# Kernel optimization log

Hardware: AMD Instinct MI355X
Metric: run time of the kernel (lower is better)

The kernel has to match this reference:

```python
import jax, jax.numpy as jnp
import numpy as np

SEQ_LEN = 8192
D_MODEL = 1024
D_K = 128
D_V = 128


def setup_inputs() -> dict:
    key = jax.random.key(0)
    kx, kq, kk, kv = jax.random.split(key, 4)
    # xavier-uniform scale for (out, in) linear weights
    def xavier(k, out_f, in_f):
        lim = np.sqrt(6.0 / (in_f + out_f))
        return jax.random.uniform(k, (out_f, in_f), jnp.float32, -lim, lim)
    return {
        "X": jax.random.normal(kx, (SEQ_LEN, D_MODEL), jnp.float32),
        "Wq": xavier(kq, D_K, D_MODEL),
        "Wk": xavier(kk, D_K, D_MODEL),
        "Wv": xavier(kv, D_V, D_MODEL),
    }


def reference(X, Wq, Wk, Wv):
    # X: (S, d_model); W*: (d_k, d_model) torch Linear weights (y = x @ W.T)
    S = X.shape[0]
    Q = X @ Wq.T                      # (S, d_k)
    K = X @ Wk.T                      # (S, d_k)
    V = X @ Wv.T                      # (S, d_v)
    scale = jnp.sqrt(jnp.asarray(D_K, X.dtype))
    scores = (Q @ K.T) / scale        # (S, S)
    causal = jnp.tril(jnp.ones((S, S), bool))
    scores = jnp.where(causal, scores, -jnp.inf)
    weights = jax.nn.softmax(scores, axis=1)
    # dropout p=0.0 -> identity
    Z = weights @ V                   # (S, d_v)
    return Z
```

## Files before the change

### kernel.cpp

```cpp
#include <hip/hip_runtime.h>
#include <hip/hip_bf16.h>

#define S_LEN 8192
#define DM    1024
#define DK    128
#define KSTR  136
#define VSTR  72
#define SLOTD 1056

typedef __attribute__((ext_vector_type(8))) short bf16x8;
typedef __attribute__((ext_vector_type(8))) _Float16 f16x8;
typedef __attribute__((ext_vector_type(4))) float f32x4;

__device__ __forceinline__ f32x4 mfma16(bf16x8 a, bf16x8 b, f32x4 c) {
    return __builtin_amdgcn_mfma_f32_16x16x32_bf16(a, b, c, 0, 0, 0);
}
__device__ __forceinline__ f32x4 mfma16f(f16x8 a, f16x8 b, f32x4 c) {
    return __builtin_amdgcn_mfma_f32_16x16x32_f16(a, b, c, 0, 0, 0);
}

__device__ __forceinline__ ushort f2bf(float f) {
    unsigned u = __builtin_bit_cast(unsigned, f);
    u += 0x7FFFu + ((u >> 16) & 1u);
    return (ushort)(u >> 16);
}

__device__ __forceinline__ ushort f2h(float f) {
    return __builtin_bit_cast(ushort, (_Float16)f);
}

__device__ __forceinline__ uint cvt_pk_bf16(float a, float b) {
    uint r;
    asm("v_cvt_pk_bf16_f32 %0, %1, %2" : "=v"(r) : "v"(a), "v"(b));
    return r;
}

__global__ __launch_bounds__(256, 1)
void convert_w_kernel(const float* __restrict__ Wq,
                      const float* __restrict__ Wk,
                      const float* __restrict__ Wv,
                      _Float16* __restrict__ Wh) {
    const int NW4 = DK * DM / 4;
    const int i = blockIdx.x * 256 + threadIdx.x;
    const int which = i / NW4;
    const int off = i - which * NW4;
    const float4 v = ((const float4*)(which == 0 ? Wq : (which == 1 ? Wk : Wv)))[off];
    union { _Float16 h[4]; uint2 u; } p;
    p.h[0] = (_Float16)v.x; p.h[1] = (_Float16)v.y;
    p.h[2] = (_Float16)v.z; p.h[3] = (_Float16)v.w;
    *(uint2*)(Wh + (size_t)which * (DK * DM) + (size_t)off * 4) = p.u;
}

__global__ __launch_bounds__(256)
void proj_gemm_kernel(const float* __restrict__ X,
                      const _Float16* __restrict__ Wh,
                      ushort* __restrict__ Qb,
                      ushort* __restrict__ Kb,
                      ushort* __restrict__ Vtb) {
    __shared__ _Float16 Ash[32 * 32];
    __shared__ _Float16 Bsh[128 * 32];

    const int tid  = threadIdx.x;
    const int lane = tid & 63;
    const int quad = lane >> 4;
    const int l15  = lane & 15;
    const int wv   = tid >> 6;
    const int wm   = wv & 1;
    const int wn   = wv >> 1;
    const int m0   = blockIdx.x * 32;
    const int nb   = blockIdx.y;
    const _Float16* Wbase = Wh + nb * (DK * DM);
    const int arow = tid >> 3, ac4 = tid & 7;

    f32x4 acc[4];
#pragma unroll
    for (int ni = 0; ni < 4; ++ni) acc[ni] = (f32x4){0.f, 0.f, 0.f, 0.f};

    float4 ra = *(const float4*)(X + (size_t)(m0 + arow) * DM + ac4 * 4);

    for (int kk = 0; kk < DM; kk += 32) {
        __syncthreads();
        for (int s = tid; s < 512; s += 256) {
            const int row = s >> 2, sg = s & 3;
            __builtin_amdgcn_global_load_lds(
                (const __attribute__((address_space(1))) void*)(Wbase + (size_t)row * DM + kk + sg * 8),
                (__attribute__((address_space(3))) void*)(Bsh + s * 8), 16, 0, 0);
        }
        {
            union { _Float16 h[4]; uint2 u; } pa;
            pa.h[0] = (_Float16)ra.x; pa.h[1] = (_Float16)ra.y;
            pa.h[2] = (_Float16)ra.z; pa.h[3] = (_Float16)ra.w;
            *(uint2*)(Ash + arow * 32 + ac4 * 4) = pa.u;
        }
        if (kk + 32 < DM)
            ra = *(const float4*)(X + (size_t)(m0 + arow) * DM + kk + 32 + ac4 * 4);
        __syncthreads();

        const f16x8 af = *(const f16x8*)(Ash + (wm * 16 + l15) * 32 + quad * 8);
        f16x8 bf[4];
#pragma unroll
        for (int t = 0; t < 4; ++t)
            bf[t] = *(const f16x8*)(Bsh + (wn * 64 + t * 16 + l15) * 32 + quad * 8);
#pragma unroll
        for (int ni = 0; ni < 4; ++ni)
            acc[ni] = mfma16f(af, bf[ni], acc[ni]);
    }

    if (nb == 2) {
#pragma unroll
        for (int ni = 0; ni < 4; ++ni) {
            const int n = wn * 64 + ni * 16 + l15;
            const int m = m0 + wm * 16 + quad * 4;
            union { ushort h[4]; uint2 u; } p;
#pragma unroll
            for (int r = 0; r < 4; ++r) p.h[r] = f2bf(acc[ni][r]);
            *(uint2*)(Vtb + (size_t)n * S_LEN + m) = p.u;
        }
    } else {
        ushort* Ob = (nb == 0) ? Qb : Kb;
        const float sc = (nb == 0) ? 0.088388347648318447f * 1.4426950408889634f : 1.0f;
#pragma unroll
        for (int ni = 0; ni < 4; ++ni) {
            const int n = wn * 64 + ni * 16 + l15;
#pragma unroll
            for (int r = 0; r < 4; ++r) {
                const int m = m0 + wm * 16 + quad * 4 + r;
                Ob[(size_t)m * DK + n] = f2bf(acc[ni][r] * sc);
            }
        }
    }
}

__global__ __launch_bounds__(256, 3)
void flash_partial_kernel(const ushort* __restrict__ Qg,
                          const ushort* __restrict__ Kg,
                          const ushort* __restrict__ Vtg,
                          float* __restrict__ Part) {
    __shared__ __align__(16) ushort Ks [64 * KSTR];
    __shared__ __align__(16) ushort Vts[128 * VSTR];

    const int b = 995 - (int)blockIdx.x;
    int qb, chunk;
    if (b < 36) {
        int q = 0;
        while (b >= (q + 1) * (q + 2) / 2) ++q;
        qb = q; chunk = b - q * (q + 1) / 2;
    } else {
        qb = 8 + ((b - 36) >> 3);
        chunk = (b - 36) & 7;
    }
    const int nkt   = qb + 1;
    const int NC    = nkt < 8 ? nkt : 8;
    const int kt_lo = chunk * nkt / NC;
    const int kt_hi = (chunk + 1) * nkt / NC;

    const int tid  = threadIdx.x;
    const int wv   = tid >> 6;
    const int lane = tid & 63;
    const int quad = lane >> 4;
    const int l15  = lane & 15;
    const int q0w  = qb * 64 + wv * 16;

    bf16x8 qf[4];
    {
        const ushort* qrow = Qg + (size_t)(q0w + l15) * DK + quad * 8;
#pragma unroll
        for (int kc = 0; kc < 4; ++kc) qf[kc] = *(const bf16x8*)(qrow + kc * 32);
    }

    float m_ = -__builtin_inff();
    float l_ = 0.f;
    f32x4 acc[8];
#pragma unroll
    for (int d = 0; d < 8; ++d) acc[d] = (f32x4){0.f, 0.f, 0.f, 0.f};

    bf16x8 stg[8];
#define LOAD_TILE(K0)                                                          \
    {                                                                          \
        const int k0_ = (K0);                                                  \
        _Pragma("unroll")                                                      \
        for (int i = 0; i < 8; ++i) {                                          \
            const int c = tid + (i << 8);                                      \
            if (c < 1024) {                                                    \
                const int row = c >> 4, ch = c & 15;                           \
                stg[i] = *(const bf16x8*)(Kg + (size_t)(k0_ + row) * DK + ch * 8); \
            } else {                                                           \
                const int cc = c - 1024;                                       \
                const int row = cc >> 3, ch = cc & 7;                          \
                stg[i] = *(const bf16x8*)(Vtg + (size_t)row * S_LEN + k0_ + ch * 8); \
            }                                                                  \
        }                                                                      \
    }

    LOAD_TILE(kt_lo * 64)

    for (int kt = kt_lo; kt < kt_hi; ++kt) {
        const int k0 = kt * 64;

        __syncthreads();
#pragma unroll
        for (int i = 0; i < 8; ++i) {
            const int c = tid + (i << 8);
            if (c < 1024) {
                const int row = c >> 4, ch = c & 15;
                *(bf16x8*)(Ks + row * KSTR + ch * 8) = stg[i];
            } else {
                const int cc = c - 1024;
                const int row = cc >> 3, ch = cc & 7;
                const int s_lo = ((ch >> 2) << 5) + ((ch & 1) << 4) + (((ch >> 1) & 1) << 2);
                union { bf16x8 v; uint2 q2[2]; } u;
                u.v = stg[i];
                ushort* vb = Vts + row * VSTR + s_lo;
                *(uint2*)vb       = u.q2[0];
                *(uint2*)(vb + 8) = u.q2[1];
            }
        }
        if (kt + 1 < kt_hi) LOAD_TILE((kt + 1) * 64)
        __syncthreads();

        f32x4 Sr[4];
        __builtin_amdgcn_s_setprio(1);
#pragma unroll
        for (int nb = 0; nb < 4; ++nb) {
            Sr[nb] = (f32x4){0.f, 0.f, 0.f, 0.f};
            const ushort* kb = Ks + (nb * 16 + l15) * KSTR + quad * 8;
#pragma unroll
            for (int kc = 0; kc < 4; ++kc)
                Sr[nb] = mfma16(*(const bf16x8*)(kb + kc * 32), qf[kc], Sr[nb]);
        }
        __builtin_amdgcn_s_setprio(0);

        if (k0 + 63 > q0w) {
            const int qg = q0w + l15;
#pragma unroll
            for (int nb = 0; nb < 4; ++nb) {
                const int kg = k0 + nb * 16 + quad * 4;
#pragma unroll
                for (int r = 0; r < 4; ++r)
                    if (kg + r > qg) Sr[nb][r] = -__builtin_inff();
            }
        }

        float pmax;
        {
            float a0 = fmaxf(fmaxf(Sr[0][0], Sr[0][1]), fmaxf(Sr[0][2], Sr[0][3]));
            float a1 = fmaxf(fmaxf(Sr[1][0], Sr[1][1]), fmaxf(Sr[1][2], Sr[1][3]));
            float a2 = fmaxf(fmaxf(Sr[2][0], Sr[2][1]), fmaxf(Sr[2][2], Sr[2][3]));
            float a3 = fmaxf(fmaxf(Sr[3][0], Sr[3][1]), fmaxf(Sr[3][2], Sr[3][3]));
            pmax = fmaxf(fmaxf(a0, a1), fmaxf(a2, a3));
            pmax = fmaxf(pmax, __shfl_xor(pmax, 16));
            pmax = fmaxf(pmax, __shfl_xor(pmax, 32));
        }
        if (__any(pmax > m_ + 8.f)) {
            const float mnew = fmaxf(m_, pmax);
            const float al = __builtin_amdgcn_exp2f(m_ - mnew);
            m_ = mnew;
            l_ *= al;
            float alr[4];
#pragma unroll
            for (int r = 0; r < 4; ++r)
                alr[r] = __shfl(al, (lane & 48) | (((lane >> 4) & 3) * 4 + r));
#pragma unroll
            for (int d = 0; d < 8; ++d)
#pragma unroll
                for (int r = 0; r < 4; ++r) acc[d][r] *= alr[r];
        }

        float p[4][4];
        float rs = 0.f;
#pragma unroll
        for (int nb = 0; nb < 4; ++nb)
#pragma unroll
            for (int r = 0; r < 4; ++r) {
                p[nb][r] = __builtin_amdgcn_exp2f(Sr[nb][r] - m_);
                rs += p[nb][r];
            }
        rs += __shfl_xor(rs, 16);
        rs += __shfl_xor(rs, 32);
        l_ += rs;

        __builtin_amdgcn_s_setprio(1);
#pragma unroll
        for (int kcp = 0; kcp < 2; ++kcp) {
            union { uint u[4]; bf16x8 v; } pf;
            pf.u[0] = cvt_pk_bf16(p[2 * kcp][0],     p[2 * kcp][1]);
            pf.u[1] = cvt_pk_bf16(p[2 * kcp][2],     p[2 * kcp][3]);
            pf.u[2] = cvt_pk_bf16(p[2 * kcp + 1][0], p[2 * kcp + 1][1]);
            pf.u[3] = cvt_pk_bf16(p[2 * kcp + 1][2], p[2 * kcp + 1][3]);
#pragma unroll
            for (int db = 0; db < 8; ++db) {
                const bf16x8 vf = *(const bf16x8*)(Vts + (db * 16 + l15) * VSTR + kcp * 32 + quad * 8);
                acc[db] = mfma16(pf.v, vf, acc[db]);
            }
        }
        __builtin_amdgcn_s_setprio(0);
    }
#undef LOAD_TILE

    const int qt16 = qb * 4 + wv;
    float* slot = Part + (size_t)(qt16 * 8 + chunk) * SLOTD;
    if (quad == 0) {
        slot[l15]      = m_;
        slot[16 + l15] = l_;
    }
    uint* slotO = (uint*)(slot + 32);
#pragma unroll
    for (int d = 0; d < 8; ++d)
#pragma unroll
        for (int r = 0; r < 4; ++r) {
            const float v  = acc[d][r];
            const float vp = __shfl_xor(v, 1);
            if ((l15 & 1) == 0) {
                const int row = quad * 4 + r;
                const uint u = (uint)f2h(v) | ((uint)f2h(vp) << 16);
                slotO[(row * 128 + d * 16 + l15) >> 1] = u;
            }
        }
}

__global__ __launch_bounds__(256)
void flash_merge_kernel(const float* __restrict__ Part, float* __restrict__ Out) {
    __shared__ float Ms[16], Ls[16];
    __shared__ float Sc[8][16];
    const int qt = blockIdx.x;
    const int q0 = qt * 16;
    const int qb = qt >> 2;
    const int P  = (qb + 1 < 8) ? (qb + 1) : 8;
    const int tid = threadIdx.x;
    const float* base = Part + (size_t)qt * 8 * SLOTD;

    if (tid < 16) {
        float M = -__builtin_inff();
        for (int p = 0; p < P; ++p) M = fmaxf(M, base[p * SLOTD + tid]);
        float L = 0.f;
        for (int p = 0; p < P; ++p)
            L += base[p * SLOTD + 16 + tid] * exp2f(base[p * SLOTD + tid] - M);
        Ms[tid] = M; Ls[tid] = L;
    }
    __syncthreads();
    if (tid < 128) {
        const int p = tid >> 4, row = tid & 15;
        Sc[p][row] = (p < P) ? exp2f(base[p * SLOTD + row] - Ms[row]) : 0.f;
    }
    __syncthreads();

#pragma unroll
    for (int j = tid; j < 1024; j += 256) {
        const int row = j >> 6, c2 = j & 63;
        float o0 = 0.f, o1 = 0.f;
        for (int p = 0; p < P; ++p) {
            const uint u = ((const uint*)(base + p * SLOTD + 32))[row * 64 + c2];
            const float sc = Sc[p][row];
            o0 += (float)__builtin_bit_cast(_Float16, (ushort)(u & 0xFFFF)) * sc;
            o1 += (float)__builtin_bit_cast(_Float16, (ushort)(u >> 16)) * sc;
        }
        const float inv = 1.0f / Ls[row];
        float2 o; o.x = o0 * inv; o.y = o1 * inv;
        *(float2*)(Out + (size_t)(q0 + row) * DK + c2 * 2) = o;
    }
}

extern "C" void kernel_launch(void* const* d_in, const int* in_sizes, int n_in,
                              void* d_out, int out_size, void* d_ws, size_t ws_size,
                              hipStream_t stream) {
    const float* X  = (const float*)d_in[0];
    const float* Wq = (const float*)d_in[1];
    const float* Wk = (const float*)d_in[2];
    const float* Wv = (const float*)d_in[3];
    ushort* ws  = (ushort*)d_ws;
    ushort* Qb  = ws;
    ushort* Kb  = ws + (size_t)S_LEN * DK;
    ushort* Vtb = ws + 2 * (size_t)S_LEN * DK;
    _Float16* Wh = (_Float16*)(ws + 3 * (size_t)S_LEN * DK);
    float* Part = (float*)(Wh + (size_t)3 * DK * DM);
    float* Out = (float*)d_out;

    convert_w_kernel<<<384, 256, 0, stream>>>(Wq, Wk, Wv, Wh);
    proj_gemm_kernel<<<dim3(256, 3), 256, 0, stream>>>(X, Wh, Qb, Kb, Vtb);
    flash_partial_kernel<<<996, 256, 0, stream>>>(Qb, Kb, Vtb, Part);
    flash_merge_kernel<<<512, 256, 0, stream>>>(Part, Out);
}
```

Before: 148.8 us.

## Register-prefetch X and W tiles with K=64 steps and padded LDS in projection GEMM

```diff
diff --git a/kernel.cpp b/kernel.cpp
--- a/kernel.cpp
+++ b/kernel.cpp
@@ -6,6 +6,7 @@
 #define DK    128
 #define KSTR  136
 #define VSTR  72
+#define ASTR  68
 #define SLOTD 1056
 
 typedef __attribute__((ext_vector_type(8))) short bf16x8;
@@ -57,8 +58,8 @@
                       ushort* __restrict__ Qb,
                       ushort* __restrict__ Kb,
                       ushort* __restrict__ Vtb) {
-    __shared__ _Float16 Ash[32 * 32];
-    __shared__ _Float16 Bsh[128 * 32];
+    __shared__ _Float16 Ash[32 * ASTR];
+    __shared__ _Float16 Bsh[128 * ASTR];
 
     const int tid  = threadIdx.x;
     const int lane = tid & 63;
@@ -70,41 +71,65 @@
     const int m0   = blockIdx.x * 32;
     const int nb   = blockIdx.y;
     const _Float16* Wbase = Wh + nb * (DK * DM);
-    const int arow = tid >> 3, ac4 = tid & 7;
 
     f32x4 acc[4];
 #pragma unroll
     for (int ni = 0; ni < 4; ++ni) acc[ni] = (f32x4){0.f, 0.f, 0.f, 0.f};
 
-    float4 ra = *(const float4*)(X + (size_t)(m0 + arow) * DM + ac4 * 4);
-
-    for (int kk = 0; kk < DM; kk += 32) {
+    float4 sa[2];
+    f16x8 sb[4];
+
+#define LOADR(KK)                                                              \
+    {                                                                          \
+        _Pragma("unroll")                                                      \
+        for (int i = 0; i < 2; ++i) {                                          \
+            const int s = tid + (i << 8);                                      \
+            sa[i] = *(const float4*)(X + (size_t)(m0 + (s >> 4)) * DM + (KK) + (s & 15) * 4); \
+        }                                                                      \
+        _Pragma("unroll")                                                      \
+        for (int i = 0; i < 4; ++i) {                                          \
+            const int s = tid + (i << 8);                                      \
+            sb[i] = *(const f16x8*)(Wbase + (size_t)(s >> 3) * DM + (KK) + (s & 7) * 8); \
+        }                                                                      \
+    }
+#define WRITE_LDS()                                                            \
+    {                                                                          \
+        _Pragma("unroll")                                                      \
+        for (int i = 0; i < 2; ++i) {                                          \
+            const int s = tid + (i << 8);                                      \
+            union { _Float16 h[4]; uint2 u; } pa_;                             \
+            pa_.h[0] = (_Float16)sa[i].x; pa_.h[1] = (_Float16)sa[i].y;        \
+            pa_.h[2] = (_Float16)sa[i].z; pa_.h[3] = (_Float16)sa[i].w;        \
+            *(uint2*)(Ash + (s >> 4) * ASTR + (s & 15) * 4) = pa_.u;           \
+        }                                                                      \
+        _Pragma("unroll")                                                      \
+        for (int i = 0; i < 4; ++i) {                                          \
+            const int s = tid + (i << 8);                                      \
+            *(f16x8*)(Bsh + (s >> 3) * ASTR + (s & 7) * 8) = sb[i];            \
+        }                                                                      \
+    }
+
+    LOADR(0)
+    for (int it = 0; it < 16; ++it) {
         __syncthreads();
-        for (int s = tid; s < 512; s += 256) {
-            const int row = s >> 2, sg = s & 3;
-            __builtin_amdgcn_global_load_lds(
-                (const __attribute__((address_space(1))) void*)(Wbase + (size_t)row * DM + kk + sg * 8),
-                (__attribute__((address_space(3))) void*)(Bsh + s * 8), 16, 0, 0);
-        }
-        {
-            union { _Float16 h[4]; uint2 u; } pa;
-            pa.h[0] = (_Float16)ra.x; pa.h[1] = (_Float16)ra.y;
-            pa.h[2] = (_Float16)ra.z; pa.h[3] = (_Float16)ra.w;
-            *(uint2*)(Ash + arow * 32 + ac4 * 4) = pa.u;
-        }
-        if (kk + 32 < DM)
-            ra = *(const float4*)(X + (size_t)(m0 + arow) * DM + kk + 32 + ac4 * 4);
+        WRITE_LDS()
+        if (it + 1 < 16) LOADR((it + 1) * 64)
         __syncthreads();
 
-        const f16x8 af = *(const f16x8*)(Ash + (wm * 16 + l15) * 32 + quad * 8);
-        f16x8 bf[4];
-#pragma unroll
-        for (int t = 0; t < 4; ++t)
-            bf[t] = *(const f16x8*)(Bsh + (wn * 64 + t * 16 + l15) * 32 + quad * 8);
-#pragma unroll
-        for (int ni = 0; ni < 4; ++ni)
-            acc[ni] = mfma16f(af, bf[ni], acc[ni]);
-    }
+        __builtin_amdgcn_s_setprio(1);
+#pragma unroll
+        for (int kc = 0; kc < 2; ++kc) {
+            const f16x8 af = *(const f16x8*)(Ash + (wm * 16 + l15) * ASTR + kc * 32 + quad * 8);
+#pragma unroll
+            for (int t = 0; t < 4; ++t) {
+                const f16x8 bf = *(const f16x8*)(Bsh + (wn * 64 + t * 16 + l15) * ASTR + kc * 32 + quad * 8);
+                acc[t] = mfma16f(af, bf, acc[t]);
+            }
+        }
+        __builtin_amdgcn_s_setprio(0);
+    }
+#undef LOADR
+#undef WRITE_LDS
 
     if (nb == 2) {
 #pragma unroll
```

After: 144.7 us (median of 2 runs). 1.03x faster.
